# Kernel tuning notes

Hardware: AMD Instinct MI355X
Metric: run time of the kernel (lower is better)

## Reference

```python
import jax, jax.numpy as jnp
import numpy as np

B, P, E, D = 256, 2048, 16, 2
HID, OUT = 128, 128
BN_EPS = 1e-5


def setup_inputs() -> dict:
    key = jax.random.key(0)
    ks = jax.random.split(key, 16)
    inp = {
        "barcode_h0": jax.random.normal(ks[0], (B, P, D), jnp.float32),
        "barcode_h0_count": jax.random.randint(ks[1], (B,), 0, P),
        "barcode_h1": jax.random.normal(ks[2], (B, P, D), jnp.float32),
        "barcode_h1_count": jax.random.randint(ks[3], (B,), 0, P),
        # SLayer params (one per homology dim): centers ~ U[0,1), log_sharpness = log(3.0)
        "centers0": jax.random.uniform(ks[4], (E, D), jnp.float32),
        "log_sharp0": jnp.full((E, D), np.log(3.0), jnp.float32),
        "centers1": jax.random.uniform(ks[5], (E, D), jnp.float32),
        "log_sharp1": jnp.full((E, D), np.log(3.0), jnp.float32),
        # head: Linear(2E -> HID, no bias), BN, ReLU, Linear(HID -> OUT, no bias), BN
        "W1": jax.random.normal(ks[6], (2 * E, HID), jnp.float32) / np.sqrt(2 * E),
        "gamma1": jnp.ones((HID,), jnp.float32),
        "beta1": jnp.zeros((HID,), jnp.float32),
        "W2": jax.random.normal(ks[7], (HID, OUT), jnp.float32) / np.sqrt(HID),
        "gamma2": jnp.ones((OUT,), jnp.float32),
        "beta2": jnp.zeros((OUT,), jnp.float32),
    }
    return inp


def _slayer(pts, counts, centers, log_sharp):
    # pts: [B,P,2], counts: [B], centers/log_sharp: [E,2]
    sharp = jax.nn.softplus(log_sharp) + 1e-6                       # [E,2]
    diff = pts[:, :, None, :] - centers[None, None, :, :]           # [B,P,E,2]
    resp = jnp.exp(-jnp.sum(sharp * diff * diff, axis=-1))          # [B,P,E]
    mask = (jnp.arange(pts.shape[1])[None, :] < counts[:, None]).astype(resp.dtype)
    return jnp.sum(resp * mask[:, :, None], axis=1)                 # [B,E]


def _batchnorm_train(x, gamma, beta):
    m = jnp.mean(x, axis=0)
    v = jnp.var(x, axis=0)  # biased, as torch uses for normalization
    return (x - m) * jax.lax.rsqrt(v + BN_EPS) * gamma + beta


def reference(barcode_h0, barcode_h0_count, barcode_h1, barcode_h1_count,
              centers0, log_sharp0, centers1, log_sharp1,
              W1, gamma1, beta1, W2, gamma2, beta2):
    f0 = _slayer(barcode_h0, barcode_h0_count, centers0, log_sharp0)  # [B,E]
    f1 = _slayer(barcode_h1, barcode_h1_count, centers1, log_sharp1)  # [B,E]
    x = jnp.concatenate([f0, f1], axis=1)                             # [B,2E]
    h = jax.nn.relu(_batchnorm_train(x @ W1, gamma1, beta1))          # [B,HID]
    y = _batchnorm_train(h @ W2, gamma2, beta2)                       # [B,OUT]
    norm = jnp.maximum(jnp.linalg.norm(y, axis=1, keepdims=True), 1e-12)
    return y / norm
```

## Files before the change

### kernel.cpp

```cpp
#include <hip/hip_runtime.h>

#define Bsz 256
#define Pn  2048
#define En  16
#define HIDn 128
#define OUTn 128
#define BN_EPS 1e-5f

__global__ __launch_bounds__(256) void k_slayer_w1(
    const float* __restrict__ pts0, const int* __restrict__ cnt0,
    const float* __restrict__ pts1, const int* __restrict__ cnt1,
    const float* __restrict__ c0, const float* __restrict__ ls0,
    const float* __restrict__ c1, const float* __restrict__ ls1,
    const float* __restrict__ W1,
    float* __restrict__ u)
{
    __shared__ float cen[2][En][2];
    __shared__ float shp[2][En][2];
    __shared__ float red[4][32];
    __shared__ float xrow[32];

    const int tid = threadIdx.x;
    const int b   = blockIdx.x;

    if (tid < 64) {
        int h = tid >> 5, r = tid & 31, e = r >> 1, d = r & 1;
        const float* C = h ? c1 : c0;
        const float* L = h ? ls1 : ls0;
        cen[h][e][d] = C[e * 2 + d];
        float z  = L[e * 2 + d];
        float sp = (z > 20.f) ? z : logf(1.f + expf(z));
        shp[h][e][d] = sp + 1e-6f;
    }
    __syncthreads();

    float acc0[En], acc1[En];
    #pragma unroll
    for (int e = 0; e < En; e++) { acc0[e] = 0.f; acc1[e] = 0.f; }

    const int n0 = cnt0[b];
    const int n1 = cnt1[b];
    const float2* p0 = (const float2*)pts0 + (size_t)b * Pn;
    const float2* p1 = (const float2*)pts1 + (size_t)b * Pn;

    for (int p = tid; p < n0; p += 256) {
        float2 pt = p0[p];
        #pragma unroll
        for (int e = 0; e < En; e++) {
            float dx = pt.x - cen[0][e][0];
            float dy = pt.y - cen[0][e][1];
            float t  = shp[0][e][0] * dx * dx + shp[0][e][1] * dy * dy;
            acc0[e] += __expf(-t);
        }
    }
    for (int p = tid; p < n1; p += 256) {
        float2 pt = p1[p];
        #pragma unroll
        for (int e = 0; e < En; e++) {
            float dx = pt.x - cen[1][e][0];
            float dy = pt.y - cen[1][e][1];
            float t  = shp[1][e][0] * dx * dx + shp[1][e][1] * dy * dy;
            acc1[e] += __expf(-t);
        }
    }

    #pragma unroll
    for (int e = 0; e < En; e++) {
        #pragma unroll
        for (int off = 32; off > 0; off >>= 1) {
            acc0[e] += __shfl_down(acc0[e], off, 64);
            acc1[e] += __shfl_down(acc1[e], off, 64);
        }
    }
    const int wave = tid >> 6, lane = tid & 63;
    if (lane == 0) {
        #pragma unroll
        for (int e = 0; e < En; e++) { red[wave][e] = acc0[e]; red[wave][16 + e] = acc1[e]; }
    }
    __syncthreads();
    if (tid < 32) xrow[tid] = red[0][tid] + red[1][tid] + red[2][tid] + red[3][tid];
    __syncthreads();

    if (tid < HIDn) {
        float a = 0.f;
        #pragma unroll
        for (int k = 0; k < 32; k++) a = fmaf(xrow[k], W1[k * HIDn + tid], a);
        u[b * HIDn + tid] = a;
    }
}

__global__ __launch_bounds__(128) void k_bn1_w2(
    const float* __restrict__ u, const float* __restrict__ W2,
    const float* __restrict__ g1, const float* __restrict__ be1,
    float* __restrict__ ypre)
{
    __shared__ float hrow[HIDn];
    const int j = threadIdx.x, b = blockIdx.x;

    float s = 0.f, sq = 0.f, uv = 0.f;
    #pragma unroll 8
    for (int bb = 0; bb < Bsz; bb++) {
        float v = u[bb * HIDn + j];
        s += v; sq = fmaf(v, v, sq);
        if (bb == b) uv = v;
    }
    float m    = s * (1.f / Bsz);
    float var  = sq * (1.f / Bsz) - m * m;
    float rstd = rsqrtf(var + BN_EPS);
    float h    = fmaxf((uv - m) * rstd * g1[j] + be1[j], 0.f);
    hrow[j] = h;
    __syncthreads();

    float a = 0.f;
    #pragma unroll 8
    for (int k = 0; k < HIDn; k++) a = fmaf(hrow[k], W2[k * OUTn + j], a);
    ypre[b * OUTn + j] = a;
}

__global__ __launch_bounds__(128) void k_bn2_norm(
    const float* __restrict__ ypre,
    const float* __restrict__ g2, const float* __restrict__ be2,
    float* __restrict__ out)
{
    __shared__ float part[2];
    const int j = threadIdx.x, b = blockIdx.x;

    float s = 0.f, sq = 0.f, yv = 0.f;
    #pragma unroll 8
    for (int bb = 0; bb < Bsz; bb++) {
        float v = ypre[bb * OUTn + j];
        s += v; sq = fmaf(v, v, sq);
        if (bb == b) yv = v;
    }
    float m    = s * (1.f / Bsz);
    float var  = sq * (1.f / Bsz) - m * m;
    float rstd = rsqrtf(var + BN_EPS);
    float y    = (yv - m) * rstd * g2[j] + be2[j];

    float s2 = y * y;
    #pragma unroll
    for (int off = 32; off > 0; off >>= 1) s2 += __shfl_down(s2, off, 64);
    if ((j & 63) == 0) part[j >> 6] = s2;
    __syncthreads();
    float total = part[0] + part[1];
    float norm  = fmaxf(sqrtf(total), 1e-12f);
    out[b * OUTn + j] = y / norm;
}

extern "C" void kernel_launch(void* const* d_in, const int* in_sizes, int n_in,
                              void* d_out, int out_size, void* d_ws, size_t ws_size,
                              hipStream_t stream) {
    const float* pts0 = (const float*)d_in[0];
    const int*   cnt0 = (const int*)  d_in[1];
    const float* pts1 = (const float*)d_in[2];
    const int*   cnt1 = (const int*)  d_in[3];
    const float* c0   = (const float*)d_in[4];
    const float* ls0  = (const float*)d_in[5];
    const float* c1   = (const float*)d_in[6];
    const float* ls1  = (const float*)d_in[7];
    const float* W1   = (const float*)d_in[8];
    const float* g1   = (const float*)d_in[9];
    const float* be1  = (const float*)d_in[10];
    const float* W2   = (const float*)d_in[11];
    const float* g2   = (const float*)d_in[12];
    const float* be2  = (const float*)d_in[13];
    float* out = (float*)d_out;

    float* ws   = (float*)d_ws;
    float* u    = ws;
    float* ypre = ws + 32768;

    k_slayer_w1<<<Bsz, 256, 0, stream>>>(pts0, cnt0, pts1, cnt1,
                                         c0, ls0, c1, ls1, W1, u);
    k_bn1_w2<<<Bsz, 128, 0, stream>>>(u, W2, g1, be1, ypre);
    k_bn2_norm<<<Bsz, 128, 0, stream>>>(ypre, g2, be2, out);
}
```

Before: 120.1 us.

## Expand Gaussian exponent into polynomial FMAs and fuse both diagrams in 512-thread blocks

Precomputes per-center coefficients so each response is four FMAs plus exp2, with log2(e) folded into the constants. Both homology diagrams are handled in one fixed, fully unrolled 4-iteration loop over all P points. Points past the count are masked by pushing x to 1e18 so the exponent underflows to zero. Blocks grow to 512 threads to raise parallelism, at the cost of always computing all 2048 points and a larger cross-wave reduction; the expanded quadratic form may lose some precision.

```diff
diff --git a/kernel.cpp b/kernel.cpp
--- a/kernel.cpp
+++ b/kernel.cpp
@@ -1,13 +1,13 @@
 #include <hip/hip_runtime.h>
 
-#define Bsz 256
-#define Pn  2048
-#define En  16
+#define Bsz  256
+#define Pn   2048
+#define En   16
 #define HIDn 128
 #define OUTn 128
 #define BN_EPS 1e-5f
 
-__global__ __launch_bounds__(256) void k_slayer_w1(
+__global__ __launch_bounds__(512) void k_slayer_w1(
     const float* __restrict__ pts0, const int* __restrict__ cnt0,
     const float* __restrict__ pts1, const int* __restrict__ cnt1,
     const float* __restrict__ c0, const float* __restrict__ ls0,
@@ -15,70 +15,87 @@
     const float* __restrict__ W1,
     float* __restrict__ u)
 {
-    __shared__ float cen[2][En][2];
-    __shared__ float shp[2][En][2];
-    __shared__ float red[4][32];
+    __shared__ float cst[2][En][5];
+    __shared__ float red[8][32];
     __shared__ float xrow[32];
 
     const int tid = threadIdx.x;
     const int b   = blockIdx.x;
 
-    if (tid < 64) {
-        int h = tid >> 5, r = tid & 31, e = r >> 1, d = r & 1;
+    if (tid < 32) {
+        int h = tid >> 4, e = tid & 15;
         const float* C = h ? c1 : c0;
         const float* L = h ? ls1 : ls0;
-        cen[h][e][d] = C[e * 2 + d];
-        float z  = L[e * 2 + d];
-        float sp = (z > 20.f) ? z : logf(1.f + expf(z));
-        shp[h][e][d] = sp + 1e-6f;
+        float cx = C[e * 2 + 0], cy = C[e * 2 + 1];
+        float z0 = L[e * 2 + 0], z1 = L[e * 2 + 1];
+        float s0 = ((z0 > 20.f) ? z0 : logf(1.f + expf(z0))) + 1e-6f;
+        float s1 = ((z1 > 20.f) ? z1 : logf(1.f + expf(z1))) + 1e-6f;
+        const float L2E = 1.44269504088896340736f;
+        float q0 = s0 * L2E, q1 = s1 * L2E;
+        cst[h][e][0] = -q0;
+        cst[h][e][1] = 2.f * q0 * cx;
+        cst[h][e][2] = -q1;
+        cst[h][e][3] = 2.f * q1 * cy;
+        cst[h][e][4] = -(q0 * cx * cx + q1 * cy * cy);
     }
     __syncthreads();
 
-    float acc0[En], acc1[En];
+    float acc[32];
     #pragma unroll
-    for (int e = 0; e < En; e++) { acc0[e] = 0.f; acc1[e] = 0.f; }
+    for (int i = 0; i < 32; i++) acc[i] = 0.f;
 
     const int n0 = cnt0[b];
     const int n1 = cnt1[b];
     const float2* p0 = (const float2*)pts0 + (size_t)b * Pn;
     const float2* p1 = (const float2*)pts1 + (size_t)b * Pn;
 
-    for (int p = tid; p < n0; p += 256) {
-        float2 pt = p0[p];
+    #pragma unroll
+    for (int k = 0; k < 4; k++) {
+        const int p = tid + k * 512;
+        float2 a = p0[p];
+        float2 c = p1[p];
+        float ax = (p < n0) ? a.x : 1e18f;
+        float ay = (p < n0) ? a.y : 0.f;
+        float cx = (p < n1) ? c.x : 1e18f;
+        float cy = (p < n1) ? c.y : 0.f;
+        float ax2 = ax * ax, ay2 = ay * ay;
+        float cx2 = cx * cx, cy2 = cy * cy;
         #pragma unroll
         for (int e = 0; e < En; e++) {
-            float dx = pt.x - cen[0][e][0];
-            float dy = pt.y - cen[0][e][1];
-            float t  = shp[0][e][0] * dx * dx + shp[0][e][1] * dy * dy;
-            acc0[e] += __expf(-t);
-        }
-    }
-    for (int p = tid; p < n1; p += 256) {
-        float2 pt = p1[p];
-        #pragma unroll
-        for (int e = 0; e < En; e++) {
-            float dx = pt.x - cen[1][e][0];
-            float dy = pt.y - cen[1][e][1];
-            float t  = shp[1][e][0] * dx * dx + shp[1][e][1] * dy * dy;
-            acc1[e] += __expf(-t);
+            float t = cst[0][e][4];
+            t = fmaf(cst[0][e][0], ax2, t);
+            t = fmaf(cst[0][e][1], ax,  t);
+            t = fmaf(cst[0][e][2], ay2, t);
+            t = fmaf(cst[0][e][3], ay,  t);
+            acc[e] += exp2f(t);
+            float s = cst[1][e][4];
+            s = fmaf(cst[1][e][0], cx2, s);
+            s = fmaf(cst[1][e][1], cx,  s);
+            s = fmaf(cst[1][e][2], cy2, s);
+            s = fmaf(cst[1][e][3], cy,  s);
+            acc[16 + e] += exp2f(s);
         }
     }
 
     #pragma unroll
-    for (int e = 0; e < En; e++) {
+    for (int i = 0; i < 32; i++) {
+        float v = acc[i];
         #pragma unroll
-        for (int off = 32; off > 0; off >>= 1) {
-            acc0[e] += __shfl_down(acc0[e], off, 64);
-            acc1[e] += __shfl_down(acc1[e], off, 64);
-        }
+        for (int off = 32; off > 0; off >>= 1) v += __shfl_down(v, off, 64);
+        acc[i] = v;
     }
     const int wave = tid >> 6, lane = tid & 63;
     if (lane == 0) {
         #pragma unroll
-        for (int e = 0; e < En; e++) { red[wave][e] = acc0[e]; red[wave][16 + e] = acc1[e]; }
+        for (int i = 0; i < 32; i++) red[wave][i] = acc[i];
     }
     __syncthreads();
-    if (tid < 32) xrow[tid] = red[0][tid] + red[1][tid] + red[2][tid] + red[3][tid];
+    if (tid < 32) {
+        float s = 0.f;
+        #pragma unroll
+        for (int w = 0; w < 8; w++) s += red[w][tid];
+        xrow[tid] = s;
+    }
     __syncthreads();
 
     if (tid < HIDn) {
@@ -170,7 +187,7 @@
     float* u    = ws;
     float* ypre = ws + 32768;
 
-    k_slayer_w1<<<Bsz, 256, 0, stream>>>(pts0, cnt0, pts1, cnt1,
+    k_slayer_w1<<<Bsz, 512, 0, stream>>>(pts0, cnt0, pts1, cnt1,
                                          c0, ls0, c1, ls1, W1, u);
     k_bn1_w2<<<Bsz, 128, 0, stream>>>(u, W2, g1, be1, ypre);
     k_bn2_norm<<<Bsz, 128, 0, stream>>>(ypre, g2, be2, out);
```

Measured after the change: 118.4 us. Within noise of the previous version (-1.5%).
